# Optimization experiments

Hardware: AMD Instinct MI355X
Metric: run time of the kernel (lower is better)

Reference implementation:

```python
import jax, jax.numpy as jnp
import numpy as np

N, E, D, H = 100000, 1000000, 128, 8
DH = D // H
SCALE = 1.0 / np.sqrt(DH)


def setup_inputs() -> dict:
    key = jax.random.key(0)
    ks = jax.random.split(key, 12)
    inp = {
        "x": jax.random.normal(ks[0], (N, D), jnp.float32),
        "edge_index": jax.random.randint(ks[1], (2, E), 0, N, dtype=jnp.int64),
        "a": jnp.array(0.25, jnp.float32),  # shared PReLU slope
    }
    names = ["Wq1", "Wk1", "Wv1", "Ws1", "Wq2", "Wk2", "Wv2", "Ws2"]
    for i, n in enumerate(names):
        # kaiming_normal_: std = sqrt(2 / fan_in)
        inp[n] = jax.random.normal(ks[2 + i], (D, D), jnp.float32) * np.sqrt(2.0 / D)
        inp["b" + n[1:]] = jnp.zeros((D,), jnp.float32)
    return inp


def prelu(x, a):
    return jnp.where(x >= 0, x, a * x)


def transformer_conv(x, src, dst, Wq, bq, Wk, bk, Wv, bv, Ws, bs):
    # PyG TransformerConv: query from target (dst), key/value from source (src),
    # scatter-softmax over incoming edges of each dst node, root skip via lin_skip.
    q = (x @ Wq + bq).reshape(N, H, DH)
    k = (x @ Wk + bk).reshape(N, H, DH)
    v = (x @ Wv + bv).reshape(N, H, DH)
    score = jnp.einsum("ehd,ehd->eh", q[dst], k[src]) * SCALE  # [E, H]
    m = jax.lax.stop_gradient(jax.ops.segment_max(score, dst, num_segments=N))  # [N, H]
    e = jnp.exp(score - m[dst])
    s = jax.ops.segment_sum(e, dst, num_segments=N)  # [N, H]
    alpha = e / s[dst]  # scatter-softmax, [E, H]
    agg = jax.ops.segment_sum(alpha[..., None] * v[src], dst, num_segments=N)  # [N, H, DH]
    return agg.reshape(N, D) + x @ Ws + bs


def reference(x, edge_index, a,
              Wq1, bq1, Wk1, bk1, Wv1, bv1, Ws1, bs1,
              Wq2, bq2, Wk2, bk2, Wv2, bv2, Ws2, bs2):
    src, dst = edge_index[0], edge_index[1]
    h = transformer_conv(x, src, dst, Wq1, bq1, Wk1, bk1, Wv1, bv1, Ws1, bs1)
    h = prelu(h, a)
    h = transformer_conv(h, src, dst, Wq2, bq2, Wk2, bk2, Wv2, bv2, Ws2, bs2)
    h = h + x
    return prelu(h, a)
```

## Files before the change

### kernel.cpp

```cpp
#include <hip/hip_runtime.h>
#include <hip/hip_bf16.h>
#include <math.h>

#define D 128
#define SCALE 0.25f
#define NEG_BIG (-1e30f)
#define SLOTS 32

typedef __attribute__((ext_vector_type(8))) short bf16x8;
typedef __attribute__((ext_vector_type(4))) float f32x4;

__device__ inline __hip_bfloat162 pack2(float a, float b) {
    __hip_bfloat162 h;
    h.x = __float2bfloat16(a);
    h.y = __float2bfloat16(b);
    return h;
}

__device__ inline int detect_is64(const int* __restrict__ ei) {
    int lane = threadIdx.x & 63;
    int v = ei[2 * lane + 1];
    unsigned long long b = __ballot(v != 0);
    return b == 0ULL;
}

struct PackArgs { const float* w[8]; };

__global__ __launch_bounds__(256) void prep(
    PackArgs pa, __hip_bfloat16* __restrict__ WtP,
    const float* __restrict__ x, __hip_bfloat16* __restrict__ xb, int n4,
    const int* __restrict__ ei, int E,
    int* __restrict__ deg, int* __restrict__ slots,
    unsigned long long* __restrict__ ovf, int* __restrict__ ovfcnt, int gE)
{
    int b = blockIdx.x;
    int tid = threadIdx.x;
    if (b < gE) {
        int is64 = detect_is64(ei);
        int e = b * 256 + tid;
        if (e < E) {
            int s = is64 ? ei[2 * e]         : ei[e];
            int d = is64 ? ei[2 * E + 2 * e] : ei[E + e];
            int pos = atomicAdd(&deg[d], 1);
            if (pos < SLOTS) {
                slots[d * SLOTS + pos] = s;
            } else {
                int op = atomicAdd(ovfcnt, 1);
                ovf[op] = ((unsigned long long)(unsigned)d << 32) | (unsigned)s;
            }
        }
    } else if (b < gE + 8) {
        int w = b - gE;
        const float* W = pa.w[w];
        __hip_bfloat16* dst = WtP + (size_t)w * 128 * 128;
        for (int idx = tid; idx < 128 * 128; idx += 256) {
            int c = idx & 127, k = idx >> 7;
            dst[(size_t)c * 128 + k] = __float2bfloat16(W[(size_t)k * 128 + c]);
        }
    } else {
        int i = (b - gE - 8) * 256 + tid;
        if (i < n4) {
            float4 v = ((const float4*)x)[i];
            ((__hip_bfloat162*)xb)[2 * i]     = pack2(v.x, v.y);
            ((__hip_bfloat162*)xb)[2 * i + 1] = pack2(v.z, v.w);
        }
    }
}

#define TSTR 136

__global__ __launch_bounds__(256) void gemm_mfma(
    const __hip_bfloat16* __restrict__ A, const __hip_bfloat16* __restrict__ Wt,
    const float* __restrict__ bq, const float* __restrict__ bk,
    const float* __restrict__ bv, const float* __restrict__ bs,
    __hip_bfloat16* __restrict__ qb, __hip_bfloat16* __restrict__ kv,
    __hip_bfloat16* __restrict__ skipb, int M)
{
    __shared__ __hip_bfloat16 bufA[64 * TSTR];
    __shared__ __hip_bfloat16 bufB[64 * TSTR];

    const int tid = threadIdx.x;
    const int w = tid >> 6, lane = tid & 63;
    const int wr = w >> 1, wc = w & 1;
    const int blk0 = blockIdx.x * 64;
    const int rowBase = blk0 + wr * 32;
    const int l16 = lane & 15;
    const int quad = lane >> 4;

    bf16x8 xfrag[2][4];
    #pragma unroll
    for (int i = 0; i < 2; ++i) {
        int r = rowBase + i * 16 + l16;
        if (r >= M) r = M - 1;
        #pragma unroll
        for (int kb = 0; kb < 4; ++kb)
            xfrag[i][kb] = *(const bf16x8*)(A + (size_t)r * D + kb * 32 + quad * 8);
    }

    const float* biases[4] = {bq, bk, bv, bs};

    for (int cb = 0; cb < 4; ++cb) {
        const __hip_bfloat16* Wblk = Wt + (size_t)cb * 128 * 128;
        f32x4 acc[2][4];
        #pragma unroll
        for (int i = 0; i < 2; i++)
            #pragma unroll
            for (int jt = 0; jt < 4; jt++) acc[i][jt] = (f32x4){0.f, 0.f, 0.f, 0.f};

        #pragma unroll
        for (int kb = 0; kb < 4; ++kb) {
            const int k0 = kb * 32 + quad * 8;
            #pragma unroll
            for (int jt = 0; jt < 4; ++jt) {
                int c = wc * 64 + jt * 16 + l16;
                bf16x8 wfrag = *(const bf16x8*)(Wblk + (size_t)c * D + k0);
                acc[0][jt] = __builtin_amdgcn_mfma_f32_16x16x32_bf16(wfrag, xfrag[0][kb], acc[0][jt], 0, 0, 0);
                acc[1][jt] = __builtin_amdgcn_mfma_f32_16x16x32_bf16(wfrag, xfrag[1][kb], acc[1][jt], 0, 0, 0);
            }
        }

        __hip_bfloat16* dst = (cb == 2) ? bufB : bufA;
        const float* bias = biases[cb];
        #pragma unroll
        for (int jt = 0; jt < 4; ++jt) {
            int c0 = wc * 64 + jt * 16 + quad * 4;
            float4 bb = *(const float4*)(bias + c0);
            #pragma unroll
            for (int i = 0; i < 2; ++i) {
                int lrow = wr * 32 + i * 16 + l16;
                f32x4 vv = acc[i][jt];
                __hip_bfloat162 h0 = pack2(vv[0] + bb.x, vv[1] + bb.y);
                __hip_bfloat162 h1 = pack2(vv[2] + bb.z, vv[3] + bb.w);
                float2 st; st.x = *(float*)&h0; st.y = *(float*)&h1;
                *(float2*)(&dst[lrow * TSTR + c0]) = st;
            }
        }

        if (cb == 1) continue;

        __syncthreads();

        if (cb == 0 || cb == 3) {
            __hip_bfloat16* gout = (cb == 0) ? qb : skipb;
            #pragma unroll
            for (int it = 0; it < 4; ++it) {
                int lrow = it * 16 + (tid >> 4);
                int grow = blk0 + lrow;
                if (grow < M) {
                    float4 vv = *(const float4*)(&bufA[lrow * TSTR + (tid & 15) * 8]);
                    *(float4*)(gout + (size_t)grow * D + (tid & 15) * 8) = vv;
                }
            }
        } else {
            #pragma unroll
            for (int it = 0; it < 8; ++it) {
                int lrow = it * 8 + (tid >> 5);
                int grow = blk0 + lrow;
                int g = tid & 31;
                if (grow < M) {
                    float2 kk = *(const float2*)(&bufA[lrow * TSTR + g * 4]);
                    float2 vv = *(const float2*)(&bufB[lrow * TSTR + g * 4]);
                    float4 o; o.x = kk.x; o.y = kk.y; o.z = vv.x; o.w = vv.y;
                    *(float4*)(kv + (size_t)grow * 256 + g * 8) = o;
                }
            }
        }
        __syncthreads();
    }
}

__device__ inline void store4(float* base, size_t off, float o0, float o1, float o2, float o3) {
    *(float4*)(base + off) = make_float4(o0, o1, o2, o3);
}
__device__ inline void store4(__hip_bfloat16* base, size_t off, float o0, float o1, float o2, float o3) {
    __hip_bfloat162 h0 = pack2(o0, o1), h1 = pack2(o2, o3);
    float2 st; st.x = *(float*)&h0; st.y = *(float*)&h1;
    *(float2*)(base + off) = st;
}

template <typename OutT>
__global__ __launch_bounds__(256) void attn_agg(
    const __hip_bfloat16* __restrict__ qb, const __hip_bfloat16* __restrict__ kv,
    const int* __restrict__ deg, const int* __restrict__ slots,
    const unsigned long long* __restrict__ ovf, const int* __restrict__ ovfcnt,
    const __hip_bfloat16* __restrict__ skip, const __hip_bfloat16* __restrict__ residb,
    const float* __restrict__ a_ptr, OutT* __restrict__ out, int Nn) {
    int tid = threadIdx.x;
    int lane = tid & 63;
    int half = lane >> 5;
    int lh = lane & 31;
    int n = blockIdx.x * 8 + (tid >> 6) * 2 + half;
    bool valid = (n < Nn);
    int nc = valid ? n : (Nn - 1);
    const float a = a_ptr[0];

    float2 qraw = *(const float2*)(qb + (size_t)nc * D + 4 * lh);
    __hip_bfloat162 q01 = *(__hip_bfloat162*)&qraw.x;
    __hip_bfloat162 q23 = *(__hip_bfloat162*)&qraw.y;
    float q0 = __bfloat162float(q01.x) * SCALE, q1 = __bfloat162float(q01.y) * SCALE;
    float q2 = __bfloat162float(q23.x) * SCALE, q3 = __bfloat162float(q23.y) * SCALE;

    float m = NEG_BIG, s = 0.f, A0 = 0.f, A1 = 0.f, A2 = 0.f, A3 = 0.f;

    int cnt = valid ? deg[nc] : 0;
    int cmain = min(cnt, SLOTS);
    int cmax = max(cmain, __shfl_xor(cmain, 32));
    int beg = nc * SLOTS;

    const float4* kvp4 = (const float4*)kv;

    for (int t = 0; t < cmax; t += 8) {
        float4 f[8];
        float sc[8];
        #pragma unroll
        for (int i = 0; i < 8; ++i) {
            int src = slots[beg + t + i];
            f[i] = kvp4[(size_t)src * 32 + lh];
        }
        #pragma unroll
        for (int i = 0; i < 8; ++i) {
            __hip_bfloat162 k01 = *(__hip_bfloat162*)&f[i].x;
            __hip_bfloat162 k23 = *(__hip_bfloat162*)&f[i].y;
            float p = q0 * __bfloat162float(k01.x) + q1 * __bfloat162float(k01.y)
                    + q2 * __bfloat162float(k23.x) + q3 * __bfloat162float(k23.y);
            p += __shfl_xor(p, 1);
            p += __shfl_xor(p, 2);
            sc[i] = (t + i < cmain) ? p : NEG_BIG;
        }
        float nm = m;
        #pragma unroll
        for (int i = 0; i < 8; ++i) nm = fmaxf(nm, sc[i]);
        float corr = __expf(m - nm);
        A0 *= corr; A1 *= corr; A2 *= corr; A3 *= corr; s *= corr;
        #pragma unroll
        for (int i = 0; i < 8; ++i) {
            float wgt = __expf(sc[i] - nm);
            __hip_bfloat162 v01 = *(__hip_bfloat162*)&f[i].z;
            __hip_bfloat162 v23 = *(__hip_bfloat162*)&f[i].w;
            A0 += wgt * __bfloat162float(v01.x);
            A1 += wgt * __bfloat162float(v01.y);
            A2 += wgt * __bfloat162float(v23.x);
            A3 += wgt * __bfloat162float(v23.y);
            s += wgt;
        }
        m = nm;
    }

    if (__any(cnt > SLOTS)) {
        int oc = *ovfcnt;
        for (int i = 0; i < oc; ++i) {
            unsigned long long e = ovf[i];
            int dd = (int)(e >> 32);
            int ss = (int)(e & 0xffffffffULL);
            bool take = (dd == nc) && (cnt > SLOTS) && valid;
            float4 fo = kvp4[(size_t)ss * 32 + lh];
            __hip_bfloat162 k01 = *(__hip_bfloat162*)&fo.x;
            __hip_bfloat162 k23 = *(__hip_bfloat162*)&fo.y;
            float p = q0 * __bfloat162float(k01.x) + q1 * __bfloat162float(k01.y)
                    + q2 * __bfloat162float(k23.x) + q3 * __bfloat162float(k23.y);
            p += __shfl_xor(p, 1);
            p += __shfl_xor(p, 2);
            float sce = take ? p : NEG_BIG;
            float nm = fmaxf(m, sce);
            float corr = __expf(m - nm);
            float wgt = take ? __expf(sce - nm) : 0.f;
            __hip_bfloat162 v01 = *(__hip_bfloat162*)&fo.z;
            __hip_bfloat162 v23 = *(__hip_bfloat162*)&fo.w;
            A0 = A0 * corr + wgt * __bfloat162float(v01.x);
            A1 = A1 * corr + wgt * __bfloat162float(v01.y);
            A2 = A2 * corr + wgt * __bfloat162float(v23.x);
            A3 = A3 * corr + wgt * __bfloat162float(v23.y);
            s = s * corr + wgt;
            m = nm;
        }
    }

    if (!valid) return;
    float inv = (cnt > 0) ? 1.f / s : 0.f;
    float2 skr = *(const float2*)(skip + (size_t)n * D + 4 * lh);
    __hip_bfloat162 s01 = *(__hip_bfloat162*)&skr.x;
    __hip_bfloat162 s23 = *(__hip_bfloat162*)&skr.y;
    float o0 = A0 * inv + __bfloat162float(s01.x);
    float o1 = A1 * inv + __bfloat162float(s01.y);
    float o2 = A2 * inv + __bfloat162float(s23.x);
    float o3 = A3 * inv + __bfloat162float(s23.y);
    if (residb) {
        float2 rr = *(const float2*)(residb + (size_t)n * D + 4 * lh);
        __hip_bfloat162 r01 = *(__hip_bfloat162*)&rr.x;
        __hip_bfloat162 r23 = *(__hip_bfloat162*)&rr.y;
        o0 += __bfloat162float(r01.x);
        o1 += __bfloat162float(r01.y);
        o2 += __bfloat162float(r23.x);
        o3 += __bfloat162float(r23.y);
    }
    o0 = (o0 >= 0.f) ? o0 : a * o0;
    o1 = (o1 >= 0.f) ? o1 : a * o1;
    o2 = (o2 >= 0.f) ? o2 : a * o2;
    o3 = (o3 >= 0.f) ? o3 : a * o3;
    store4(out, (size_t)n * D + 4 * lh, o0, o1, o2, o3);
}

extern "C" void kernel_launch(void* const* d_in, const int* in_sizes, int n_in,
                              void* d_out, int out_size, void* d_ws, size_t ws_size,
                              hipStream_t stream) {
    const float* x  = (const float*)d_in[0];
    const int*   ei = (const int*)d_in[1];
    const float* a  = (const float*)d_in[2];
    const float* Wq1 = (const float*)d_in[3];  const float* bq1 = (const float*)d_in[4];
    const float* Wk1 = (const float*)d_in[5];  const float* bk1 = (const float*)d_in[6];
    const float* Wv1 = (const float*)d_in[7];  const float* bv1 = (const float*)d_in[8];
    const float* Ws1 = (const float*)d_in[9];  const float* bs1 = (const float*)d_in[10];
    const float* Wq2 = (const float*)d_in[11]; const float* bq2 = (const float*)d_in[12];
    const float* Wk2 = (const float*)d_in[13]; const float* bk2 = (const float*)d_in[14];
    const float* Wv2 = (const float*)d_in[15]; const float* bv2 = (const float*)d_in[16];
    const float* Ws2 = (const float*)d_in[17]; const float* bs2 = (const float*)d_in[18];

    const int N = in_sizes[0] / D;
    const int E = in_sizes[1] / 2;
    const size_t NF = (size_t)N * D;

    char* wp = (char*)d_ws;
    __hip_bfloat16* xb    = (__hip_bfloat16*)wp; wp += NF * 2;
    __hip_bfloat16* h1b   = (__hip_bfloat16*)wp; wp += NF * 2;
    __hip_bfloat16* qb    = (__hip_bfloat16*)wp; wp += NF * 2;
    __hip_bfloat16* kv    = (__hip_bfloat16*)wp; wp += NF * 4;
    __hip_bfloat16* skipb = (__hip_bfloat16*)wp; wp += NF * 2;
    __hip_bfloat16* WtP   = (__hip_bfloat16*)wp; wp += 2 * 512 * 128 * 2;
    int* deg    = (int*)wp;                wp += (size_t)N * 4;
    int* ovfcnt = (int*)wp;                wp += 64;
    int* slots  = (int*)wp;                wp += (size_t)N * SLOTS * 4;
    size_t zbytes = (size_t)N * 4 + 64 + (size_t)N * SLOTS * 4;
    unsigned long long* ovf = (unsigned long long*)wp; wp += (size_t)E * 8;
    float* out = (float*)d_out;

    const int TB = 256;
    int gE = (E + TB - 1) / TB;
    int gGemm = (N + 63) / 64;
    int gAttn = (N + 7) / 8;
    int n4 = (int)(NF / 4);
    int gCvt = (n4 + TB - 1) / TB;

    PackArgs pa;
    pa.w[0] = Wq1; pa.w[1] = Wk1; pa.w[2] = Wv1; pa.w[3] = Ws1;
    pa.w[4] = Wq2; pa.w[5] = Wk2; pa.w[6] = Wv2; pa.w[7] = Ws2;

    hipMemsetAsync(deg, 0, zbytes, stream);
    hipLaunchKernelGGL(prep, dim3(gE + 8 + gCvt), dim3(TB), 0, stream,
                       pa, WtP, x, xb, n4, ei, E, deg, slots, ovf, ovfcnt, gE);

    hipLaunchKernelGGL(gemm_mfma, dim3(gGemm), dim3(TB), 0, stream,
                       xb, WtP, bq1, bk1, bv1, bs1, qb, kv, skipb, N);
    hipLaunchKernelGGL(attn_agg<__hip_bfloat16>, dim3(gAttn), dim3(TB), 0, stream,
                       qb, kv, deg, slots, ovf, ovfcnt, skipb,
                       (const __hip_bfloat16*)nullptr, a, h1b, N);

    hipLaunchKernelGGL(gemm_mfma, dim3(gGemm), dim3(TB), 0, stream,
                       h1b, WtP + 512 * 128, bq2, bk2, bv2, bs2, qb, kv, skipb, N);
    hipLaunchKernelGGL(attn_agg<float>, dim3(gAttn), dim3(TB), 0, stream,
                       qb, kv, deg, slots, ovf, ovfcnt, skipb, xb, a, out, N);
}
```

Baseline: 524.8 us.

## Fuse edge scatter into first GEMM kernel and stop zeroing slot table

Moves the edge bucketing (degree atomics and slot writes) out of the prep kernel and into the first MFMA GEMM kernel, with each GEMM block handling a contiguous chunk of edges before it runs its GEMM tile. The memset no longer clears the large N*32 slot array, only the degree counters and overflow count. Because stale slot entries may now be read past the valid count, the attention kernel clamps source indices to the valid range. The intent is to overlap the latency-bound atomic scatter with GEMM work and to cut memset bandwidth, at the cost of serializing scatter ahead of the GEMM inside each block.

```diff
diff --git a/kernel.cpp b/kernel.cpp
--- a/kernel.cpp
+++ b/kernel.cpp
@@ -26,39 +26,21 @@
 
 struct PackArgs { const float* w[8]; };
 
-__global__ __launch_bounds__(256) void prep(
+__global__ __launch_bounds__(256) void prep_light(
     PackArgs pa, __hip_bfloat16* __restrict__ WtP,
-    const float* __restrict__ x, __hip_bfloat16* __restrict__ xb, int n4,
-    const int* __restrict__ ei, int E,
-    int* __restrict__ deg, int* __restrict__ slots,
-    unsigned long long* __restrict__ ovf, int* __restrict__ ovfcnt, int gE)
+    const float* __restrict__ x, __hip_bfloat16* __restrict__ xb, int n4)
 {
     int b = blockIdx.x;
     int tid = threadIdx.x;
-    if (b < gE) {
-        int is64 = detect_is64(ei);
-        int e = b * 256 + tid;
-        if (e < E) {
-            int s = is64 ? ei[2 * e]         : ei[e];
-            int d = is64 ? ei[2 * E + 2 * e] : ei[E + e];
-            int pos = atomicAdd(&deg[d], 1);
-            if (pos < SLOTS) {
-                slots[d * SLOTS + pos] = s;
-            } else {
-                int op = atomicAdd(ovfcnt, 1);
-                ovf[op] = ((unsigned long long)(unsigned)d << 32) | (unsigned)s;
-            }
-        }
-    } else if (b < gE + 8) {
-        int w = b - gE;
-        const float* W = pa.w[w];
-        __hip_bfloat16* dst = WtP + (size_t)w * 128 * 128;
+    if (b < 8) {
+        const float* W = pa.w[b];
+        __hip_bfloat16* dst = WtP + (size_t)b * 128 * 128;
         for (int idx = tid; idx < 128 * 128; idx += 256) {
             int c = idx & 127, k = idx >> 7;
             dst[(size_t)c * 128 + k] = __float2bfloat16(W[(size_t)k * 128 + c]);
         }
     } else {
-        int i = (b - gE - 8) * 256 + tid;
+        int i = (b - 8) * 256 + tid;
         if (i < n4) {
             float4 v = ((const float4*)x)[i];
             ((__hip_bfloat162*)xb)[2 * i]     = pack2(v.x, v.y);
@@ -69,20 +51,18 @@
 
 #define TSTR 136
 
-__global__ __launch_bounds__(256) void gemm_mfma(
+__device__ __forceinline__ void gemm_body(
+    int bx, __hip_bfloat16* bufA, __hip_bfloat16* bufB,
     const __hip_bfloat16* __restrict__ A, const __hip_bfloat16* __restrict__ Wt,
     const float* __restrict__ bq, const float* __restrict__ bk,
     const float* __restrict__ bv, const float* __restrict__ bs,
     __hip_bfloat16* __restrict__ qb, __hip_bfloat16* __restrict__ kv,
     __hip_bfloat16* __restrict__ skipb, int M)
 {
-    __shared__ __hip_bfloat16 bufA[64 * TSTR];
-    __shared__ __hip_bfloat16 bufB[64 * TSTR];
-
     const int tid = threadIdx.x;
     const int w = tid >> 6, lane = tid & 63;
     const int wr = w >> 1, wc = w & 1;
-    const int blk0 = blockIdx.x * 64;
+    const int blk0 = bx * 64;
     const int rowBase = blk0 + wr * 32;
     const int l16 = lane & 15;
     const int quad = lane >> 4;
@@ -167,6 +147,50 @@
         }
         __syncthreads();
     }
+}
+
+__global__ __launch_bounds__(256) void gemm_mfma(
+    const __hip_bfloat16* __restrict__ A, const __hip_bfloat16* __restrict__ Wt,
+    const float* __restrict__ bq, const float* __restrict__ bk,
+    const float* __restrict__ bv, const float* __restrict__ bs,
+    __hip_bfloat16* __restrict__ qb, __hip_bfloat16* __restrict__ kv,
+    __hip_bfloat16* __restrict__ skipb, int M)
+{
+    __shared__ __hip_bfloat16 bufA[64 * TSTR];
+    __shared__ __hip_bfloat16 bufB[64 * TSTR];
+    gemm_body(blockIdx.x, bufA, bufB, A, Wt, bq, bk, bv, bs, qb, kv, skipb, M);
+}
+
+__global__ __launch_bounds__(256) void scatter_gemm1(
+    const __hip_bfloat16* __restrict__ A, const __hip_bfloat16* __restrict__ Wt,
+    const float* __restrict__ bq, const float* __restrict__ bk,
+    const float* __restrict__ bv, const float* __restrict__ bs,
+    __hip_bfloat16* __restrict__ qb, __hip_bfloat16* __restrict__ kv,
+    __hip_bfloat16* __restrict__ skipb, int M,
+    const int* __restrict__ ei, int E, int EPB,
+    int* __restrict__ deg, int* __restrict__ slots,
+    unsigned long long* __restrict__ ovf, int* __restrict__ ovfcnt)
+{
+    __shared__ __hip_bfloat16 bufA[64 * TSTR];
+    __shared__ __hip_bfloat16 bufB[64 * TSTR];
+
+    {
+        int is64 = detect_is64(ei);
+        int base = blockIdx.x * EPB;
+        int lim = base + EPB; if (lim > E) lim = E;
+        for (int e = base + threadIdx.x; e < lim; e += 256) {
+            int s = is64 ? ei[2 * e]         : ei[e];
+            int d = is64 ? ei[2 * E + 2 * e] : ei[E + e];
+            int pos = atomicAdd(&deg[d], 1);
+            if (pos < SLOTS) {
+                slots[d * SLOTS + pos] = s;
+            } else {
+                int op = atomicAdd(ovfcnt, 1);
+                ovf[op] = ((unsigned long long)(unsigned)d << 32) | (unsigned)s;
+            }
+        }
+    }
+    gemm_body(blockIdx.x, bufA, bufB, A, Wt, bq, bk, bv, bs, qb, kv, skipb, M);
 }
 
 __device__ inline void store4(float* base, size_t off, float o0, float o1, float o2, float o3) {
@@ -215,6 +239,7 @@
         #pragma unroll
         for (int i = 0; i < 8; ++i) {
             int src = slots[beg + t + i];
+            src = ((unsigned)src < (unsigned)Nn) ? src : 0;
             f[i] = kvp4[(size_t)src * 32 + lh];
         }
         #pragma unroll
@@ -253,6 +278,7 @@
             int dd = (int)(e >> 32);
             int ss = (int)(e & 0xffffffffULL);
             bool take = (dd == nc) && (cnt > SLOTS) && valid;
+            ss = ((unsigned)ss < (unsigned)Nn) ? ss : 0;
             float4 fo = kvp4[(size_t)ss * 32 + lh];
             __hip_bfloat162 k01 = *(__hip_bfloat162*)&fo.x;
             __hip_bfloat162 k23 = *(__hip_bfloat162*)&fo.y;
@@ -328,28 +354,29 @@
     __hip_bfloat16* WtP   = (__hip_bfloat16*)wp; wp += 2 * 512 * 128 * 2;
     int* deg    = (int*)wp;                wp += (size_t)N * 4;
     int* ovfcnt = (int*)wp;                wp += 64;
+    size_t zbytes = (size_t)N * 4 + 64;
     int* slots  = (int*)wp;                wp += (size_t)N * SLOTS * 4;
-    size_t zbytes = (size_t)N * 4 + 64 + (size_t)N * SLOTS * 4;
     unsigned long long* ovf = (unsigned long long*)wp; wp += (size_t)E * 8;
     float* out = (float*)d_out;
 
     const int TB = 256;
-    int gE = (E + TB - 1) / TB;
     int gGemm = (N + 63) / 64;
     int gAttn = (N + 7) / 8;
     int n4 = (int)(NF / 4);
     int gCvt = (n4 + TB - 1) / TB;
+    int EPB = (E + gGemm - 1) / gGemm;
 
     PackArgs pa;
     pa.w[0] = Wq1; pa.w[1] = Wk1; pa.w[2] = Wv1; pa.w[3] = Ws1;
     pa.w[4] = Wq2; pa.w[5] = Wk2; pa.w[6] = Wv2; pa.w[7] = Ws2;
 
     hipMemsetAsync(deg, 0, zbytes, stream);
-    hipLaunchKernelGGL(prep, dim3(gE + 8 + gCvt), dim3(TB), 0, stream,
-                       pa, WtP, x, xb, n4, ei, E, deg, slots, ovf, ovfcnt, gE);
-
-    hipLaunchKernelGGL(gemm_mfma, dim3(gGemm), dim3(TB), 0, stream,
-                       xb, WtP, bq1, bk1, bv1, bs1, qb, kv, skipb, N);
+    hipLaunchKernelGGL(prep_light, dim3(8 + gCvt), dim3(TB), 0, stream,
+                       pa, WtP, x, xb, n4);
+
+    hipLaunchKernelGGL(scatter_gemm1, dim3(gGemm), dim3(TB), 0, stream,
+                       xb, WtP, bq1, bk1, bv1, bs1, qb, kv, skipb, N,
+                       ei, E, EPB, deg, slots, ovf, ovfcnt);
     hipLaunchKernelGGL(attn_agg<__hip_bfloat16>, dim3(gAttn), dim3(TB), 0, stream,
                        qb, kv, deg, slots, ovf, ovfcnt, skipb,
                        (const __hip_bfloat16*)nullptr, a, h1b, N);
```

New measurement: 516.4 us. No clear change (-1.6%).
